# Kernel optimization log

Hardware: AMD Instinct MI355X
Metric: run time of the kernel (lower is better)

## Reference

```python
import jax, jax.numpy as jnp
import numpy as np

B, T, D_IN, H, LAT = 256, 512, 32, 128, 64


def lstm_scan(x, Wih, Whh, bih, bhh):
    """PyTorch-convention single-layer LSTM over x [B,T,D] -> hidden states [B,T,H].
    Gate order: i, f, g, o. Gates = x@Wih.T + bih + h@Whh.T + bhh."""
    Bm, _, _ = x.shape
    Hm = Whh.shape[1]
    # precompute input contributions for all timesteps: [B,T,4H]
    xg = jnp.einsum('btd,gd->btg', x, Wih) + bih + bhh

    def step(carry, g_t):
        h, c = carry
        gates = g_t + h @ Whh.T  # [B,4H]
        i, f, g, o = jnp.split(gates, 4, axis=-1)
        i = jax.nn.sigmoid(i)
        f = jax.nn.sigmoid(f)
        g = jnp.tanh(g)
        o = jax.nn.sigmoid(o)
        c = f * c + i * g
        h = o * jnp.tanh(c)
        return (h, c), h

    h0 = jnp.zeros((Bm, Hm), x.dtype)
    (_, _), hs = jax.lax.scan(step, (h0, h0), jnp.swapaxes(xg, 0, 1))
    return jnp.swapaxes(hs, 0, 1)  # [B,T,H]


def setup_inputs() -> dict:
    key = jax.random.key(0)
    ks = jax.random.split(key, 14)
    s = 1.0 / np.sqrt(H)

    def u(k, shape):
        return jax.random.uniform(k, shape, jnp.float32, -s, s)

    return {
        'x': jax.random.normal(ks[0], (B, T, D_IN), jnp.float32),
        # encoder LSTM (input_dim -> hidden)
        'enc_Wih': u(ks[1], (4 * H, D_IN)),
        'enc_Whh': u(ks[2], (4 * H, H)),
        'enc_bih': u(ks[3], (4 * H,)),
        'enc_bhh': u(ks[4], (4 * H,)),
        # encoder linear (hidden -> latent)
        'enc_Wl': u(ks[5], (LAT, H)),
        'enc_bl': u(ks[6], (LAT,)),
        # decoder LSTM (latent -> hidden)
        'dec_Wih': u(ks[7], (4 * H, LAT)),
        'dec_Whh': u(ks[8], (4 * H, H)),
        'dec_bih': u(ks[9], (4 * H,)),
        'dec_bhh': u(ks[10], (4 * H,)),
        # decoder linear (hidden -> input_dim)
        'dec_Wl': u(ks[11], (D_IN, H)),
        'dec_bl': u(ks[12], (D_IN,)),
    }


def reference(x, enc_Wih, enc_Whh, enc_bih, enc_bhh, enc_Wl, enc_bl,
              dec_Wih, dec_Whh, dec_bih, dec_bhh, dec_Wl, dec_bl):
    # Encoder: last hidden state -> linear -> latent
    hs = lstm_scan(x, enc_Wih, enc_Whh, enc_bih, enc_bhh)  # [B,T,H]
    h_last = hs[:, -1]                                     # == hidden.squeeze(0)
    encoded = h_last @ enc_Wl.T + enc_bl                   # [B,LAT]
    # Decoder: repeat latent over time, LSTM, linear
    z = jnp.broadcast_to(encoded[:, None, :], (encoded.shape[0], T, encoded.shape[1]))
    hs2 = lstm_scan(z, dec_Wih, dec_Whh, dec_bih, dec_bhh)  # [B,T,H]
    decoded = hs2 @ dec_Wl.T + dec_bl                       # [B,T,D_IN]
    return encoded, decoded
```

## Files before the change

### kernel.cpp

```cpp
#include <hip/hip_runtime.h>

#define NB   256
#define NT   512
#define NDIN 32
#define NH   128
#define NLAT 64
#define HSTR 136

typedef _Float16 f16x8 __attribute__((ext_vector_type(8)));
typedef float    f32x4 __attribute__((ext_vector_type(4)));
typedef _Float16 h2    __attribute__((ext_vector_type(2)));
typedef _Float16 h4    __attribute__((ext_vector_type(4)));

__device__ __forceinline__ float dot2(h2 a, h2 b, float c) {
  return __builtin_amdgcn_fdot2(a, b, c, false);
}
__device__ __forceinline__ h2 bc2(float v) { return __builtin_bit_cast(h2, v); }
__device__ __forceinline__ h2 pk2(float a, float b) { return h2{(_Float16)a, (_Float16)b}; }

#define NLOG2E 1.44269504f
__device__ __forceinline__ float sigmoid_f(float x) {
  return __builtin_amdgcn_rcpf(1.f + __builtin_amdgcn_exp2f(x * -NLOG2E));
}
__device__ __forceinline__ float tanh_f(float x) {
  float s = __builtin_amdgcn_rcpf(1.f + __builtin_amdgcn_exp2f(x * (-2.f * NLOG2E)));
  return fmaf(2.f, s, -1.f);
}
__device__ __forceinline__ f32x4 mfma16(f16x8 a, f16x8 b, f32x4 c) {
  return __builtin_amdgcn_mfma_f32_16x16x32_f16(a, b, c, 0, 0, 0);
}

template <int CTRL>
__device__ __forceinline__ float dpp_mov(float v) {
  int p = __builtin_amdgcn_update_dpp(0, __builtin_bit_cast(int, v),
                                      CTRL, 0xF, 0xF, true);
  return __builtin_bit_cast(float, p);
}
#define ROR4  0x124
#define ROR8  0x128
#define ROR12 0x12C

__global__ __launch_bounds__(512, 1) void lstm_ae_kernel(
    const float* __restrict__ x,
    const float* __restrict__ eWih,
    const float* __restrict__ eWhh,
    const float* __restrict__ eBih,
    const float* __restrict__ eBhh,
    const float* __restrict__ eWl,
    const float* __restrict__ eBl,
    const float* __restrict__ dWih,
    const float* __restrict__ dWhh,
    const float* __restrict__ dBih,
    const float* __restrict__ dBhh,
    const float* __restrict__ dWl,
    const float* __restrict__ dBl,
    float* __restrict__ outE,
    float* __restrict__ outD)
{
  extern __shared__ __align__(16) char smem[];
  float*    encs = (float*)smem;
  _Float16* hs   = (_Float16*)(encs + NLAT);
  _Float16* hist = hs + 2 * NH;
  _Float16* xs   = hist;
  float*    gtmp = (float*)(hist + NT * HSTR);

  const int tid = threadIdx.x;
  const int b   = blockIdx.x;
  const int w   = tid >> 6;
  const int l   = tid & 63;
  const int m   = l & 15;
  const int kg  = l >> 4;
  const int ag  = m & 3;
  const int ar  = 2 * (m >> 2);

  int au[4], cu[4];
#pragma unroll
  for (int tt = 0; tt < 4; ++tt) {
    au[tt] = 16 * w + 8 * (tt >> 1) + ar + (tt & 1);
    cu[tt] = 16 * w + 8 * (tt >> 1) + 2 * kg + (tt & 1);
  }
  const bool sb0 = (l & 1) != 0, sb1 = (l & 2) != 0;
  const bool b2  = (l & 4) != 0, b3  = (l & 8) != 0;
  const int  cu_sel = 16 * w + 8 * ((l >> 1) & 1) + 2 * kg + (l & 1);
  const bool writer = (l & 12) == 0;
  const bool gthn   = b3 && !b2;
  const float km = gthn ? (-2.f * NLOG2E) : -NLOG2E;
  const float pa = gthn ? 2.f : 1.f;
  const float pb = gthn ? -1.f : 0.f;

  {
    const float4* xg = (const float4*)(x + (size_t)b * (NT * NDIN));
    h4* xo = (h4*)xs;
#pragma unroll
    for (int i = 0; i < 8; ++i) {
      int idx = i * 512 + tid;
      float4 v = xg[idx];
      xo[idx] = h4{(_Float16)v.x, (_Float16)v.y, (_Float16)v.z, (_Float16)v.w};
    }
  }

  f16x8 aw[4][4];
  f16x8 ax[4];
  f32x4 bi[4];
#pragma unroll
  for (int tt = 0; tt < 4; ++tt) {
    const float* r = eWhh + (size_t)(ag * NH + au[tt]) * NH;
#pragma unroll
    for (int K = 0; K < 4; ++K) {
      const float* p = r + 32 * K + 8 * kg;
#pragma unroll
      for (int j = 0; j < 8; ++j) aw[tt][K][j] = (_Float16)p[j];
    }
    const float* q = eWih + (size_t)(ag * NH + au[tt]) * NDIN + 8 * kg;
#pragma unroll
    for (int j = 0; j < 8; ++j) ax[tt][j] = (_Float16)q[j];
#pragma unroll
    for (int j = 0; j < 4; ++j)
      bi[tt][j] = eBih[j * NH + cu[tt]] + eBhh[j * NH + cu[tt]];
  }
  if (tid < 2 * NH) hs[tid] = (_Float16)0.f;
  float c = 0.f;
  __syncthreads();

#pragma unroll 1
  for (int t = 0; t < NT; ++t) {
    f32x4 acc[4];
    const _Float16* hb = hs + (t & 1) * NH;
    {
      f16x8 bf = *(const f16x8*)(hb + 8 * kg);
#pragma unroll
      for (int tt = 0; tt < 4; ++tt) acc[tt] = mfma16(aw[tt][0], bf, bi[tt]);
    }
#pragma unroll
    for (int K = 1; K < 4; ++K) {
      f16x8 bf = *(const f16x8*)(hb + 32 * K + 8 * kg);
#pragma unroll
      for (int tt = 0; tt < 4; ++tt) acc[tt] = mfma16(aw[tt][K], bf, acc[tt]);
    }
    {
      f16x8 xf = *(const f16x8*)(xs + t * NDIN + 8 * kg);
#pragma unroll
      for (int tt = 0; tt < 4; ++tt) acc[tt] = mfma16(ax[tt], xf, acc[tt]);
    }
    float z;
    {
      float v0, v1, v2, v3;
      {
        float u0 = b3 ? acc[0][2] : acc[0][0], u1 = b3 ? acc[0][3] : acc[0][1];
        v0 = b2 ? u1 : u0;
      }
      {
        float u0 = b3 ? acc[1][2] : acc[1][0], u1 = b3 ? acc[1][3] : acc[1][1];
        v1 = b2 ? u1 : u0;
      }
      {
        float u0 = b3 ? acc[2][2] : acc[2][0], u1 = b3 ? acc[2][3] : acc[2][1];
        v2 = b2 ? u1 : u0;
      }
      {
        float u0 = b3 ? acc[3][2] : acc[3][0], u1 = b3 ? acc[3][3] : acc[3][1];
        v3 = b2 ? u1 : u0;
      }
      float w0 = sb1 ? v2 : v0, w1 = sb1 ? v3 : v1;
      z = sb0 ? w1 : w0;
    }
    float a = fmaf(pa, __builtin_amdgcn_rcpf(1.f + __builtin_amdgcn_exp2f(z * km)), pb);
    float vf = dpp_mov<ROR12>(a);
    float vg = dpp_mov<ROR8>(a);
    float vo = dpp_mov<ROR4>(a);
    c = fmaf(vf, c, a * vg);
    float h = vo * tanh_f(c);
    if (writer) hs[((t + 1) & 1) * NH + cu_sel] = (_Float16)h;
    __syncthreads();
  }

  if (tid < NLAT) {
    const float4* p  = (const float4*)(eWl + (size_t)tid * NH);
    const float2* hh = (const float2*)hs;
    float a = eBl[tid];
#pragma unroll
    for (int r = 0; r < 32; ++r) {
      float4 wv = p[r];
      float2 hp = hh[r];
      h2 lov = bc2(hp.x), hiv = bc2(hp.y);
      a = fmaf((float)lov.x, wv.x, a); a = fmaf((float)lov.y, wv.y, a);
      a = fmaf((float)hiv.x, wv.z, a); a = fmaf((float)hiv.y, wv.w, a);
    }
    encs[tid] = a;
    outE[b * NLAT + tid] = a;
  }
#pragma unroll
  for (int tt = 0; tt < 4; ++tt) {
    const float* r = dWhh + (size_t)(ag * NH + au[tt]) * NH;
#pragma unroll
    for (int K = 0; K < 4; ++K) {
      const float* p = r + 32 * K + 8 * kg;
#pragma unroll
      for (int j = 0; j < 8; ++j) aw[tt][K][j] = (_Float16)p[j];
    }
  }
  __syncthreads();

  if (tid < 2 * NH) hs[tid] = (_Float16)0.f;
  {
    const float4* p  = (const float4*)(dWih + (size_t)tid * NLAT);
    const float4* e4 = (const float4*)encs;
    float a = dBih[tid] + dBhh[tid];
#pragma unroll
    for (int r = 0; r < 16; ++r) {
      float4 wv = p[r]; float4 ev = e4[r];
      a = fmaf(ev.x, wv.x, a); a = fmaf(ev.y, wv.y, a);
      a = fmaf(ev.z, wv.z, a); a = fmaf(ev.w, wv.w, a);
    }
    gtmp[tid] = a;
  }
  __syncthreads();
#pragma unroll
  for (int tt = 0; tt < 4; ++tt) {
#pragma unroll
    for (int j = 0; j < 4; ++j) bi[tt][j] = gtmp[j * NH + cu[tt]];
  }
  c = 0.f;

#pragma unroll 1
  for (int t = 0; t < NT; ++t) {
    f32x4 acc[4];
    const _Float16* hb = hs + (t & 1) * NH;
    {
      f16x8 bf = *(const f16x8*)(hb + 8 * kg);
#pragma unroll
      for (int tt = 0; tt < 4; ++tt) acc[tt] = mfma16(aw[tt][0], bf, bi[tt]);
    }
#pragma unroll
    for (int K = 1; K < 4; ++K) {
      f16x8 bf = *(const f16x8*)(hb + 32 * K + 8 * kg);
#pragma unroll
      for (int tt = 0; tt < 4; ++tt) acc[tt] = mfma16(aw[tt][K], bf, acc[tt]);
    }
    float z;
    {
      float v0, v1, v2, v3;
      {
        float u0 = b3 ? acc[0][2] : acc[0][0], u1 = b3 ? acc[0][3] : acc[0][1];
        v0 = b2 ? u1 : u0;
      }
      {
        float u0 = b3 ? acc[1][2] : acc[1][0], u1 = b3 ? acc[1][3] : acc[1][1];
        v1 = b2 ? u1 : u0;
      }
      {
        float u0 = b3 ? acc[2][2] : acc[2][0], u1 = b3 ? acc[2][3] : acc[2][1];
        v2 = b2 ? u1 : u0;
      }
      {
        float u0 = b3 ? acc[3][2] : acc[3][0], u1 = b3 ? acc[3][3] : acc[3][1];
        v3 = b2 ? u1 : u0;
      }
      float w0 = sb1 ? v2 : v0, w1 = sb1 ? v3 : v1;
      z = sb0 ? w1 : w0;
    }
    float a = fmaf(pa, __builtin_amdgcn_rcpf(1.f + __builtin_amdgcn_exp2f(z * km)), pb);
    float vf = dpp_mov<ROR12>(a);
    float vg = dpp_mov<ROR8>(a);
    float vo = dpp_mov<ROR4>(a);
    c = fmaf(vf, c, a * vg);
    float h = vo * tanh_f(c);
    if (writer) {
      _Float16 hh = (_Float16)h;
      hs[((t + 1) & 1) * NH + cu_sel] = hh;
      hist[t * HSTR + cu_sel] = hh;
    }
    __syncthreads();
  }

  {
    const int col = tid & 31, rg = tid >> 5;
    h2 wl[64];
    const float4* p0 = (const float4*)(dWl + (size_t)col * NH);
#pragma unroll
    for (int f = 0; f < 32; ++f) {
      float4 v = p0[f];
      wl[2 * f] = pk2(v.x, v.y); wl[2 * f + 1] = pk2(v.z, v.w);
    }
    const float bo = dBl[col];
    float* op = outD + (size_t)b * (NT * NDIN);
#pragma unroll 1
    for (int i = 0; i < 32; ++i) {
      int r = rg + 16 * i;
      const float4* hp = (const float4*)(hist + r * HSTR);
      float s = 0.f;
#pragma unroll
      for (int j = 0; j < 16; ++j) {
        float4 hvv = hp[j];
        s = dot2(wl[4 * j + 0], bc2(hvv.x), s);
        s = dot2(wl[4 * j + 1], bc2(hvv.y), s);
        s = dot2(wl[4 * j + 2], bc2(hvv.z), s);
        s = dot2(wl[4 * j + 3], bc2(hvv.w), s);
      }
      op[(size_t)r * NDIN + col] = s + bo;
    }
  }
}

#define SMEM_BYTES (NLAT * 4 + 2 * NH * 2 + NT * HSTR * 2 + 512 * 4)

extern "C" void kernel_launch(void* const* d_in, const int* in_sizes, int n_in,
                              void* d_out, int out_size, void* d_ws, size_t ws_size,
                              hipStream_t stream) {
  const float* x    = (const float*)d_in[0];
  const float* eWih = (const float*)d_in[1];
  const float* eWhh = (const float*)d_in[2];
  const float* eBih = (const float*)d_in[3];
  const float* eBhh = (const float*)d_in[4];
  const float* eWl  = (const float*)d_in[5];
  const float* eBl  = (const float*)d_in[6];
  const float* dWih = (const float*)d_in[7];
  const float* dWhh = (const float*)d_in[8];
  const float* dBih = (const float*)d_in[9];
  const float* dBhh = (const float*)d_in[10];
  const float* dWl  = (const float*)d_in[11];
  const float* dBl  = (const float*)d_in[12];

  float* outE = (float*)d_out;
  float* outD = outE + (size_t)NB * NLAT;

  (void)hipFuncSetAttribute((const void*)lstm_ae_kernel,
                            hipFuncAttributeMaxDynamicSharedMemorySize,
                            SMEM_BYTES);

  hipLaunchKernelGGL(lstm_ae_kernel, dim3(NB), dim3(512), SMEM_BYTES, stream,
                     x, eWih, eWhh, eBih, eBhh, eWl, eBl,
                     dWih, dWhh, dBih, dBhh, dWl, dBl, outE, outD);
}
```

Measured before the change: 598.2 us.

## Replace MFMA recurrent matvec with per-thread fdot2 dot products and quad DPP reductions

Measured after the change: 625.1 us. +4.5%, slower.

```diff
diff --git a/kernel.cpp b/kernel.cpp
--- a/kernel.cpp
+++ b/kernel.cpp
@@ -7,7 +7,6 @@
 #define NLAT 64
 #define HSTR 136
 
-typedef _Float16 f16x8 __attribute__((ext_vector_type(8)));
 typedef float    f32x4 __attribute__((ext_vector_type(4)));
 typedef _Float16 h2    __attribute__((ext_vector_type(2)));
 typedef _Float16 h4    __attribute__((ext_vector_type(4)));
@@ -19,15 +18,9 @@
 __device__ __forceinline__ h2 pk2(float a, float b) { return h2{(_Float16)a, (_Float16)b}; }
 
 #define NLOG2E 1.44269504f
-__device__ __forceinline__ float sigmoid_f(float x) {
-  return __builtin_amdgcn_rcpf(1.f + __builtin_amdgcn_exp2f(x * -NLOG2E));
-}
 __device__ __forceinline__ float tanh_f(float x) {
   float s = __builtin_amdgcn_rcpf(1.f + __builtin_amdgcn_exp2f(x * (-2.f * NLOG2E)));
   return fmaf(2.f, s, -1.f);
-}
-__device__ __forceinline__ f32x4 mfma16(f16x8 a, f16x8 b, f32x4 c) {
-  return __builtin_amdgcn_mfma_f32_16x16x32_f16(a, b, c, 0, 0, 0);
 }
 
 template <int CTRL>
@@ -36,9 +29,13 @@
                                       CTRL, 0xF, 0xF, true);
   return __builtin_bit_cast(float, p);
 }
-#define ROR4  0x124
-#define ROR8  0x128
-#define ROR12 0x12C
+#define QXOR1 0xB1
+#define QXOR2 0x4E
+#define QP1   0x39
+#define QP2   0x4E
+#define QP3   0x93
+template <int CTRL>
+__device__ __forceinline__ float qadd(float v) { return v + dpp_mov<CTRL>(v); }
 
 __global__ __launch_bounds__(512, 1) void lstm_ae_kernel(
     const float* __restrict__ x,
@@ -66,27 +63,15 @@
 
   const int tid = threadIdx.x;
   const int b   = blockIdx.x;
-  const int w   = tid >> 6;
-  const int l   = tid & 63;
-  const int m   = l & 15;
-  const int kg  = l >> 4;
-  const int ag  = m & 3;
-  const int ar  = 2 * (m >> 2);
-
-  int au[4], cu[4];
-#pragma unroll
-  for (int tt = 0; tt < 4; ++tt) {
-    au[tt] = 16 * w + 8 * (tt >> 1) + ar + (tt & 1);
-    cu[tt] = 16 * w + 8 * (tt >> 1) + 2 * kg + (tt & 1);
-  }
-  const bool sb0 = (l & 1) != 0, sb1 = (l & 2) != 0;
-  const bool b2  = (l & 4) != 0, b3  = (l & 8) != 0;
-  const int  cu_sel = 16 * w + 8 * ((l >> 1) & 1) + 2 * kg + (l & 1);
-  const bool writer = (l & 12) == 0;
-  const bool gthn   = b3 && !b2;
-  const float km = gthn ? (-2.f * NLOG2E) : -NLOG2E;
-  const float pa = gthn ? 2.f : 1.f;
-  const float pb = gthn ? -1.f : 0.f;
+  const int u   = tid >> 2;
+  const int kc  = tid & 3;
+  const bool writer = (kc == 0);
+  const bool k0 = (kc & 1) != 0;
+  const bool k1 = (kc & 2) != 0;
+  const bool gth = (kc == 2);
+  const float km = gth ? (-2.f * NLOG2E) : -NLOG2E;
+  const float pa = gth ? 2.f : 1.f;
+  const float pb = gth ? -1.f : 0.f;
 
   {
     const float4* xg = (const float4*)(x + (size_t)b * (NT * NDIN));
@@ -99,24 +84,26 @@
     }
   }
 
-  f16x8 aw[4][4];
-  f16x8 ax[4];
-  f32x4 bi[4];
-#pragma unroll
-  for (int tt = 0; tt < 4; ++tt) {
-    const float* r = eWhh + (size_t)(ag * NH + au[tt]) * NH;
-#pragma unroll
-    for (int K = 0; K < 4; ++K) {
-      const float* p = r + 32 * K + 8 * kg;
-#pragma unroll
-      for (int j = 0; j < 8; ++j) aw[tt][K][j] = (_Float16)p[j];
-    }
-    const float* q = eWih + (size_t)(ag * NH + au[tt]) * NDIN + 8 * kg;
-#pragma unroll
-    for (int j = 0; j < 8; ++j) ax[tt][j] = (_Float16)q[j];
-#pragma unroll
-    for (int j = 0; j < 4; ++j)
-      bi[tt][j] = eBih[j * NH + cu[tt]] + eBhh[j * NH + cu[tt]];
+  h2 ew[64], dw[64], ewih[16];
+  float binit[4];
+#pragma unroll
+  for (int g = 0; g < 4; ++g) {
+    const int r = g * NH + u;
+    const float4* p = (const float4*)(eWhh + (size_t)r * NH + 32 * kc);
+#pragma unroll
+    for (int j = 0; j < 8; ++j) {
+      float4 v = p[j];
+      ew[g * 16 + 2 * j]     = pk2(v.x, v.y);
+      ew[g * 16 + 2 * j + 1] = pk2(v.z, v.w);
+    }
+    const float4* q = (const float4*)(eWih + (size_t)r * NDIN + 8 * kc);
+    float4 v0 = q[0], v1 = q[1];
+    ewih[g * 4 + 0] = pk2(v0.x, v0.y);
+    ewih[g * 4 + 1] = pk2(v0.z, v0.w);
+    ewih[g * 4 + 2] = pk2(v1.x, v1.y);
+    ewih[g * 4 + 3] = pk2(v1.z, v1.w);
+    float bsum = eBih[r] + eBhh[r];
+    binit[g] = writer ? bsum : 0.f;
   }
   if (tid < 2 * NH) hs[tid] = (_Float16)0.f;
   float c = 0.f;
@@ -124,53 +111,47 @@
 
 #pragma unroll 1
   for (int t = 0; t < NT; ++t) {
-    f32x4 acc[4];
-    const _Float16* hb = hs + (t & 1) * NH;
-    {
-      f16x8 bf = *(const f16x8*)(hb + 8 * kg);
-#pragma unroll
-      for (int tt = 0; tt < 4; ++tt) acc[tt] = mfma16(aw[tt][0], bf, bi[tt]);
-    }
-#pragma unroll
-    for (int K = 1; K < 4; ++K) {
-      f16x8 bf = *(const f16x8*)(hb + 32 * K + 8 * kg);
-#pragma unroll
-      for (int tt = 0; tt < 4; ++tt) acc[tt] = mfma16(aw[tt][K], bf, acc[tt]);
-    }
-    {
-      f16x8 xf = *(const f16x8*)(xs + t * NDIN + 8 * kg);
-#pragma unroll
-      for (int tt = 0; tt < 4; ++tt) acc[tt] = mfma16(ax[tt], xf, acc[tt]);
-    }
-    float z;
-    {
-      float v0, v1, v2, v3;
-      {
-        float u0 = b3 ? acc[0][2] : acc[0][0], u1 = b3 ? acc[0][3] : acc[0][1];
-        v0 = b2 ? u1 : u0;
-      }
-      {
-        float u0 = b3 ? acc[1][2] : acc[1][0], u1 = b3 ? acc[1][3] : acc[1][1];
-        v1 = b2 ? u1 : u0;
-      }
-      {
-        float u0 = b3 ? acc[2][2] : acc[2][0], u1 = b3 ? acc[2][3] : acc[2][1];
-        v2 = b2 ? u1 : u0;
-      }
-      {
-        float u0 = b3 ? acc[3][2] : acc[3][0], u1 = b3 ? acc[3][3] : acc[3][1];
-        v3 = b2 ? u1 : u0;
-      }
-      float w0 = sb1 ? v2 : v0, w1 = sb1 ? v3 : v1;
-      z = sb0 ? w1 : w0;
-    }
-    float a = fmaf(pa, __builtin_amdgcn_rcpf(1.f + __builtin_amdgcn_exp2f(z * km)), pb);
-    float vf = dpp_mov<ROR12>(a);
-    float vg = dpp_mov<ROR8>(a);
-    float vo = dpp_mov<ROR4>(a);
+    const float4* hp = (const float4*)(hs + (t & 1) * NH + 32 * kc);
+    float4 h0 = hp[0], h1 = hp[1], h2v = hp[2], h3 = hp[3];
+    float4 xv = *(const float4*)(xs + t * NDIN + 8 * kc);
+    float zz[4];
+#pragma unroll
+    for (int g = 0; g < 4; ++g) {
+      float A = binit[g];
+      A = dot2(ew[g * 16 +  0], bc2(h0.x), A);
+      A = dot2(ew[g * 16 +  1], bc2(h0.y), A);
+      A = dot2(ew[g * 16 +  2], bc2(h0.z), A);
+      A = dot2(ew[g * 16 +  3], bc2(h0.w), A);
+      A = dot2(ew[g * 16 +  4], bc2(h1.x), A);
+      A = dot2(ew[g * 16 +  5], bc2(h1.y), A);
+      A = dot2(ew[g * 16 +  6], bc2(h1.z), A);
+      A = dot2(ew[g * 16 +  7], bc2(h1.w), A);
+      A = dot2(ew[g * 16 +  8], bc2(h2v.x), A);
+      A = dot2(ew[g * 16 +  9], bc2(h2v.y), A);
+      A = dot2(ew[g * 16 + 10], bc2(h2v.z), A);
+      A = dot2(ew[g * 16 + 11], bc2(h2v.w), A);
+      A = dot2(ew[g * 16 + 12], bc2(h3.x), A);
+      A = dot2(ew[g * 16 + 13], bc2(h3.y), A);
+      A = dot2(ew[g * 16 + 14], bc2(h3.z), A);
+      A = dot2(ew[g * 16 + 15], bc2(h3.w), A);
+      A = dot2(ewih[g * 4 + 0], bc2(xv.x), A);
+      A = dot2(ewih[g * 4 + 1], bc2(xv.y), A);
+      A = dot2(ewih[g * 4 + 2], bc2(xv.z), A);
+      A = dot2(ewih[g * 4 + 3], bc2(xv.w), A);
+      A = qadd<QXOR1>(A);
+      A = qadd<QXOR2>(A);
+      zz[g] = A;
+    }
+    float zl = k0 ? zz[1] : zz[0];
+    float zh = k0 ? zz[3] : zz[2];
+    float z  = k1 ? zh : zl;
+    float a  = fmaf(pa, __builtin_amdgcn_rcpf(1.f + __builtin_amdgcn_exp2f(z * km)), pb);
+    float vf = dpp_mov<QP1>(a);
+    float vg = dpp_mov<QP2>(a);
+    float vo = dpp_mov<QP3>(a);
     c = fmaf(vf, c, a * vg);
     float h = vo * tanh_f(c);
-    if (writer) hs[((t + 1) & 1) * NH + cu_sel] = (_Float16)h;
+    if (writer) hs[((t + 1) & 1) * NH + u] = (_Float16)h;
     __syncthreads();
   }
 
@@ -190,13 +171,14 @@
     outE[b * NLAT + tid] = a;
   }
 #pragma unroll
-  for (int tt = 0; tt < 4; ++tt) {
-    const float* r = dWhh + (size_t)(ag * NH + au[tt]) * NH;
-#pragma unroll
-    for (int K = 0; K < 4; ++K) {
-      const float* p = r + 32 * K + 8 * kg;
-#pragma unroll
-      for (int j = 0; j < 8; ++j) aw[tt][K][j] = (_Float16)p[j];
+  for (int g = 0; g < 4; ++g) {
+    const int r = g * NH + u;
+    const float4* p = (const float4*)(dWhh + (size_t)r * NH + 32 * kc);
+#pragma unroll
+    for (int j = 0; j < 8; ++j) {
+      float4 v = p[j];
+      dw[g * 16 + 2 * j]     = pk2(v.x, v.y);
+      dw[g * 16 + 2 * j + 1] = pk2(v.z, v.w);
     }
   }
   __syncthreads();
@@ -215,60 +197,53 @@
     gtmp[tid] = a;
   }
   __syncthreads();
-#pragma unroll
-  for (int tt = 0; tt < 4; ++tt) {
-#pragma unroll
-    for (int j = 0; j < 4; ++j) bi[tt][j] = gtmp[j * NH + cu[tt]];
-  }
+  float dinit[4];
+#pragma unroll
+  for (int g = 0; g < 4; ++g)
+    dinit[g] = writer ? gtmp[g * NH + u] : 0.f;
   c = 0.f;
 
 #pragma unroll 1
   for (int t = 0; t < NT; ++t) {
-    f32x4 acc[4];
-    const _Float16* hb = hs + (t & 1) * NH;
-    {
-      f16x8 bf = *(const f16x8*)(hb + 8 * kg);
-#pragma unroll
-      for (int tt = 0; tt < 4; ++tt) acc[tt] = mfma16(aw[tt][0], bf, bi[tt]);
-    }
-#pragma unroll
-    for (int K = 1; K < 4; ++K) {
-      f16x8 bf = *(const f16x8*)(hb + 32 * K + 8 * kg);
-#pragma unroll
-      for (int tt = 0; tt < 4; ++tt) acc[tt] = mfma16(aw[tt][K], bf, acc[tt]);
-    }
-    float z;
-    {
-      float v0, v1, v2, v3;
-      {
-        float u0 = b3 ? acc[0][2] : acc[0][0], u1 = b3 ? acc[0][3] : acc[0][1];
-        v0 = b2 ? u1 : u0;
-      }
-      {
-        float u0 = b3 ? acc[1][2] : acc[1][0], u1 = b3 ? acc[1][3] : acc[1][1];
-        v1 = b2 ? u1 : u0;
-      }
-      {
-        float u0 = b3 ? acc[2][2] : acc[2][0], u1 = b3 ? acc[2][3] : acc[2][1];
-        v2 = b2 ? u1 : u0;
-      }
-      {
-        float u0 = b3 ? acc[3][2] : acc[3][0], u1 = b3 ? acc[3][3] : acc[3][1];
-        v3 = b2 ? u1 : u0;
-      }
-      float w0 = sb1 ? v2 : v0, w1 = sb1 ? v3 : v1;
-      z = sb0 ? w1 : w0;
-    }
-    float a = fmaf(pa, __builtin_amdgcn_rcpf(1.f + __builtin_amdgcn_exp2f(z * km)), pb);
-    float vf = dpp_mov<ROR12>(a);
-    float vg = dpp_mov<ROR8>(a);
-    float vo = dpp_mov<ROR4>(a);
+    const float4* hp = (const float4*)(hs + (t & 1) * NH + 32 * kc);
+    float4 h0 = hp[0], h1 = hp[1], h2v = hp[2], h3 = hp[3];
+    float zz[4];
+#pragma unroll
+    for (int g = 0; g < 4; ++g) {
+      float A = dinit[g];
+      A = dot2(dw[g * 16 +  0], bc2(h0.x), A);
+      A = dot2(dw[g * 16 +  1], bc2(h0.y), A);
+      A = dot2(dw[g * 16 +  2], bc2(h0.z), A);
+      A = dot2(dw[g * 16 +  3], bc2(h0.w), A);
+      A = dot2(dw[g * 16 +  4], bc2(h1.x), A);
+      A = dot2(dw[g * 16 +  5], bc2(h1.y), A);
+      A = dot2(dw[g * 16 +  6], bc2(h1.z), A);
+      A = dot2(dw[g * 16 +  7], bc2(h1.w), A);
+      A = dot2(dw[g * 16 +  8], bc2(h2v.x), A);
+      A = dot2(dw[g * 16 +  9], bc2(h2v.y), A);
+      A = dot2(dw[g * 16 + 10], bc2(h2v.z), A);
+      A = dot2(dw[g * 16 + 11], bc2(h2v.w), A);
+      A = dot2(dw[g * 16 + 12], bc2(h3.x), A);
+      A = dot2(dw[g * 16 + 13], bc2(h3.y), A);
+      A = dot2(dw[g * 16 + 14], bc2(h3.z), A);
+      A = dot2(dw[g * 16 + 15], bc2(h3.w), A);
+      A = qadd<QXOR1>(A);
+      A = qadd<QXOR2>(A);
+      zz[g] = A;
+    }
+    float zl = k0 ? zz[1] : zz[0];
+    float zh = k0 ? zz[3] : zz[2];
+    float z  = k1 ? zh : zl;
+    float a  = fmaf(pa, __builtin_amdgcn_rcpf(1.f + __builtin_amdgcn_exp2f(z * km)), pb);
+    float vf = dpp_mov<QP1>(a);
+    float vg = dpp_mov<QP2>(a);
+    float vo = dpp_mov<QP3>(a);
     c = fmaf(vf, c, a * vg);
     float h = vo * tanh_f(c);
     if (writer) {
       _Float16 hh = (_Float16)h;
-      hs[((t + 1) & 1) * NH + cu_sel] = hh;
-      hist[t * HSTR + cu_sel] = hh;
+      hs[((t + 1) & 1) * NH + u] = hh;
+      hist[t * HSTR + u] = hh;
     }
     __syncthreads();
   }
```

## Split LSTM recurrence between MFMA waves and VALU dot2 waves

Applied to the files above, without the earlier changes.

New measurement: 719.6 us. +20.3%, slower.

```diff
diff --git a/kernel.cpp b/kernel.cpp
--- a/kernel.cpp
+++ b/kernel.cpp
@@ -17,17 +17,14 @@
 }
 __device__ __forceinline__ h2 bc2(float v) { return __builtin_bit_cast(h2, v); }
 __device__ __forceinline__ h2 pk2(float a, float b) { return h2{(_Float16)a, (_Float16)b}; }
+__device__ __forceinline__ f32x4 mfma16(f16x8 a, f16x8 b, f32x4 c) {
+  return __builtin_amdgcn_mfma_f32_16x16x32_f16(a, b, c, 0, 0, 0);
+}
 
 #define NLOG2E 1.44269504f
-__device__ __forceinline__ float sigmoid_f(float x) {
-  return __builtin_amdgcn_rcpf(1.f + __builtin_amdgcn_exp2f(x * -NLOG2E));
-}
 __device__ __forceinline__ float tanh_f(float x) {
   float s = __builtin_amdgcn_rcpf(1.f + __builtin_amdgcn_exp2f(x * (-2.f * NLOG2E)));
   return fmaf(2.f, s, -1.f);
-}
-__device__ __forceinline__ f32x4 mfma16(f16x8 a, f16x8 b, f32x4 c) {
-  return __builtin_amdgcn_mfma_f32_16x16x32_f16(a, b, c, 0, 0, 0);
 }
 
 template <int CTRL>
@@ -39,6 +36,13 @@
 #define ROR4  0x124
 #define ROR8  0x128
 #define ROR12 0x12C
+#define QXOR1 0xB1
+#define QXOR2 0x4E
+#define QP1   0x39
+#define QP2   0x4E
+#define QP3   0x93
+template <int CTRL>
+__device__ __forceinline__ float qadd(float v) { return v + dpp_mov<CTRL>(v); }
 
 __global__ __launch_bounds__(512, 1) void lstm_ae_kernel(
     const float* __restrict__ x,
@@ -68,25 +72,36 @@
   const int b   = blockIdx.x;
   const int w   = tid >> 6;
   const int l   = tid & 63;
+  const bool is_mfma = (w < 4);
+
   const int m   = l & 15;
   const int kg  = l >> 4;
   const int ag  = m & 3;
   const int ar  = 2 * (m >> 2);
-
   int au[4], cu[4];
 #pragma unroll
   for (int tt = 0; tt < 4; ++tt) {
     au[tt] = 16 * w + 8 * (tt >> 1) + ar + (tt & 1);
     cu[tt] = 16 * w + 8 * (tt >> 1) + 2 * kg + (tt & 1);
   }
-  const bool sb0 = (l & 1) != 0, sb1 = (l & 2) != 0;
-  const bool b2  = (l & 4) != 0, b3  = (l & 8) != 0;
+  const bool ts0 = (l & 1) != 0, ts1 = (l & 2) != 0;
+  const bool gb2 = (l & 4) != 0, gb3 = (l & 8) != 0;
   const int  cu_sel = 16 * w + 8 * ((l >> 1) & 1) + 2 * kg + (l & 1);
-  const bool writer = (l & 12) == 0;
-  const bool gthn   = b3 && !b2;
-  const float km = gthn ? (-2.f * NLOG2E) : -NLOG2E;
-  const float pa = gthn ? 2.f : 1.f;
-  const float pb = gthn ? -1.f : 0.f;
+  const bool writer0 = (l & 12) == 0;
+  const bool gthn    = gb3 && !gb2;
+  const float km0 = gthn ? (-2.f * NLOG2E) : -NLOG2E;
+  const float pa0 = gthn ? 2.f : 1.f;
+  const float pb0 = gthn ? -1.f : 0.f;
+
+  const int u   = tid >> 2;
+  const int kc  = tid & 3;
+  const bool writer1 = (kc == 0);
+  const bool k0 = (kc & 1) != 0;
+  const bool k1 = (kc & 2) != 0;
+  const bool gthv = (kc == 2);
+  const float km1 = gthv ? (-2.f * NLOG2E) : -NLOG2E;
+  const float pa1 = gthv ? 2.f : 1.f;
+  const float pb1 = gthv ? -1.f : 0.f;
 
   {
     const float4* xg = (const float4*)(x + (size_t)b * (NT * NDIN));
@@ -102,21 +117,45 @@
   f16x8 aw[4][4];
   f16x8 ax[4];
   f32x4 bi[4];
-#pragma unroll
-  for (int tt = 0; tt < 4; ++tt) {
-    const float* r = eWhh + (size_t)(ag * NH + au[tt]) * NH;
-#pragma unroll
-    for (int K = 0; K < 4; ++K) {
-      const float* p = r + 32 * K + 8 * kg;
-#pragma unroll
-      for (int j = 0; j < 8; ++j) aw[tt][K][j] = (_Float16)p[j];
-    }
-    const float* q = eWih + (size_t)(ag * NH + au[tt]) * NDIN + 8 * kg;
-#pragma unroll
-    for (int j = 0; j < 8; ++j) ax[tt][j] = (_Float16)q[j];
-#pragma unroll
-    for (int j = 0; j < 4; ++j)
-      bi[tt][j] = eBih[j * NH + cu[tt]] + eBhh[j * NH + cu[tt]];
+  h2 ew[64], ewih[16];
+  float binit[4];
+  if (is_mfma) {
+#pragma unroll
+    for (int tt = 0; tt < 4; ++tt) {
+      const float* r = eWhh + (size_t)(ag * NH + au[tt]) * NH;
+#pragma unroll
+      for (int K = 0; K < 4; ++K) {
+        const float* p = r + 32 * K + 8 * kg;
+#pragma unroll
+        for (int j = 0; j < 8; ++j) aw[tt][K][j] = (_Float16)p[j];
+      }
+      const float* q = eWih + (size_t)(ag * NH + au[tt]) * NDIN + 8 * kg;
+#pragma unroll
+      for (int j = 0; j < 8; ++j) ax[tt][j] = (_Float16)q[j];
+#pragma unroll
+      for (int j = 0; j < 4; ++j)
+        bi[tt][j] = eBih[j * NH + cu[tt]] + eBhh[j * NH + cu[tt]];
+    }
+  } else {
+#pragma unroll
+    for (int g = 0; g < 4; ++g) {
+      const int r = g * NH + u;
+      const float4* p = (const float4*)(eWhh + (size_t)r * NH + 32 * kc);
+#pragma unroll
+      for (int j = 0; j < 8; ++j) {
+        float4 v = p[j];
+        ew[g * 16 + 2 * j]     = pk2(v.x, v.y);
+        ew[g * 16 + 2 * j + 1] = pk2(v.z, v.w);
+      }
+      const float4* q = (const float4*)(eWih + (size_t)r * NDIN + 8 * kc);
+      float4 v0 = q[0], v1 = q[1];
+      ewih[g * 4 + 0] = pk2(v0.x, v0.y);
+      ewih[g * 4 + 1] = pk2(v0.z, v0.w);
+      ewih[g * 4 + 2] = pk2(v1.x, v1.y);
+      ewih[g * 4 + 3] = pk2(v1.z, v1.w);
+      float bsum = eBih[r] + eBhh[r];
+      binit[g] = writer1 ? bsum : 0.f;
+    }
   }
   if (tid < 2 * NH) hs[tid] = (_Float16)0.f;
   float c = 0.f;
@@ -124,53 +163,85 @@
 
 #pragma unroll 1
   for (int t = 0; t < NT; ++t) {
-    f32x4 acc[4];
     const _Float16* hb = hs + (t & 1) * NH;
-    {
-      f16x8 bf = *(const f16x8*)(hb + 8 * kg);
-#pragma unroll
-      for (int tt = 0; tt < 4; ++tt) acc[tt] = mfma16(aw[tt][0], bf, bi[tt]);
-    }
-#pragma unroll
-    for (int K = 1; K < 4; ++K) {
-      f16x8 bf = *(const f16x8*)(hb + 32 * K + 8 * kg);
-#pragma unroll
-      for (int tt = 0; tt < 4; ++tt) acc[tt] = mfma16(aw[tt][K], bf, acc[tt]);
-    }
-    {
-      f16x8 xf = *(const f16x8*)(xs + t * NDIN + 8 * kg);
-#pragma unroll
-      for (int tt = 0; tt < 4; ++tt) acc[tt] = mfma16(ax[tt], xf, acc[tt]);
-    }
-    float z;
-    {
-      float v0, v1, v2, v3;
+    if (is_mfma) {
+      f32x4 acc[4];
       {
-        float u0 = b3 ? acc[0][2] : acc[0][0], u1 = b3 ? acc[0][3] : acc[0][1];
-        v0 = b2 ? u1 : u0;
+        f16x8 bf = *(const f16x8*)(hb + 8 * kg);
+#pragma unroll
+        for (int tt = 0; tt < 4; ++tt) acc[tt] = mfma16(aw[tt][0], bf, bi[tt]);
+      }
+#pragma unroll
+      for (int K = 1; K < 4; ++K) {
+        f16x8 bf = *(const f16x8*)(hb + 32 * K + 8 * kg);
+#pragma unroll
+        for (int tt = 0; tt < 4; ++tt) acc[tt] = mfma16(aw[tt][K], bf, acc[tt]);
       }
       {
-        float u0 = b3 ? acc[1][2] : acc[1][0], u1 = b3 ? acc[1][3] : acc[1][1];
-        v1 = b2 ? u1 : u0;
-      }
+        f16x8 xf = *(const f16x8*)(xs + t * NDIN + 8 * kg);
+#pragma unroll
+        for (int tt = 0; tt < 4; ++tt) acc[tt] = mfma16(ax[tt], xf, acc[tt]);
+      }
+      float z;
       {
-        float u0 = b3 ? acc[2][2] : acc[2][0], u1 = b3 ? acc[2][3] : acc[2][1];
-        v2 = b2 ? u1 : u0;
-      }
-      {
-        float u0 = b3 ? acc[3][2] : acc[3][0], u1 = b3 ? acc[3][3] : acc[3][1];
-        v3 = b2 ? u1 : u0;
-      }
-      float w0 = sb1 ? v2 : v0, w1 = sb1 ? v3 : v1;
-      z = sb0 ? w1 : w0;
-    }
-    float a = fmaf(pa, __builtin_amdgcn_rcpf(1.f + __builtin_amdgcn_exp2f(z * km)), pb);
-    float vf = dpp_mov<ROR12>(a);
-    float vg = dpp_mov<ROR8>(a);
-    float vo = dpp_mov<ROR4>(a);
-    c = fmaf(vf, c, a * vg);
-    float h = vo * tanh_f(c);
-    if (writer) hs[((t + 1) & 1) * NH + cu_sel] = (_Float16)h;
+        float v0, v1, v2, v3;
+        { float u0 = gb3 ? acc[0][2] : acc[0][0], u1 = gb3 ? acc[0][3] : acc[0][1]; v0 = gb2 ? u1 : u0; }
+        { float u0 = gb3 ? acc[1][2] : acc[1][0], u1 = gb3 ? acc[1][3] : acc[1][1]; v1 = gb2 ? u1 : u0; }
+        { float u0 = gb3 ? acc[2][2] : acc[2][0], u1 = gb3 ? acc[2][3] : acc[2][1]; v2 = gb2 ? u1 : u0; }
+        { float u0 = gb3 ? acc[3][2] : acc[3][0], u1 = gb3 ? acc[3][3] : acc[3][1]; v3 = gb2 ? u1 : u0; }
+        float w0 = ts1 ? v2 : v0, w1 = ts1 ? v3 : v1;
+        z = ts0 ? w1 : w0;
+      }
+      float a = fmaf(pa0, __builtin_amdgcn_rcpf(1.f + __builtin_amdgcn_exp2f(z * km0)), pb0);
+      float vf = dpp_mov<ROR12>(a);
+      float vg = dpp_mov<ROR8>(a);
+      float vo = dpp_mov<ROR4>(a);
+      c = fmaf(vf, c, a * vg);
+      float h = vo * tanh_f(c);
+      if (writer0) hs[((t + 1) & 1) * NH + cu_sel] = (_Float16)h;
+    } else {
+      const float4* hp = (const float4*)(hb + 32 * kc);
+      float4 h0 = hp[0], h1 = hp[1], h2v = hp[2], h3 = hp[3];
+      float4 xv = *(const float4*)(xs + t * NDIN + 8 * kc);
+      float zz[4];
+#pragma unroll
+      for (int g = 0; g < 4; ++g) {
+        float A = binit[g];
+        A = dot2(ew[g * 16 +  0], bc2(h0.x), A);
+        A = dot2(ew[g * 16 +  1], bc2(h0.y), A);
+        A = dot2(ew[g * 16 +  2], bc2(h0.z), A);
+        A = dot2(ew[g * 16 +  3], bc2(h0.w), A);
+        A = dot2(ew[g * 16 +  4], bc2(h1.x), A);
+        A = dot2(ew[g * 16 +  5], bc2(h1.y), A);
+        A = dot2(ew[g * 16 +  6], bc2(h1.z), A);
+        A = dot2(ew[g * 16 +  7], bc2(h1.w), A);
+        A = dot2(ew[g * 16 +  8], bc2(h2v.x), A);
+        A = dot2(ew[g * 16 +  9], bc2(h2v.y), A);
+        A = dot2(ew[g * 16 + 10], bc2(h2v.z), A);
+        A = dot2(ew[g * 16 + 11], bc2(h2v.w), A);
+        A = dot2(ew[g * 16 + 12], bc2(h3.x), A);
+        A = dot2(ew[g * 16 + 13], bc2(h3.y), A);
+        A = dot2(ew[g * 16 + 14], bc2(h3.z), A);
+        A = dot2(ew[g * 16 + 15], bc2(h3.w), A);
+        A = dot2(ewih[g * 4 + 0], bc2(xv.x), A);
+        A = dot2(ewih[g * 4 + 1], bc2(xv.y), A);
+        A = dot2(ewih[g * 4 + 2], bc2(xv.z), A);
+        A = dot2(ewih[g * 4 + 3], bc2(xv.w), A);
+        A = qadd<QXOR1>(A);
+        A = qadd<QXOR2>(A);
+        zz[g] = A;
+      }
+      float zl = k0 ? zz[1] : zz[0];
+      float zh = k0 ? zz[3] : zz[2];
+      float z  = k1 ? zh : zl;
+      float a  = fmaf(pa1, __builtin_amdgcn_rcpf(1.f + __builtin_amdgcn_exp2f(z * km1)), pb1);
+      float vf = dpp_mov<QP1>(a);
+      float vg = dpp_mov<QP2>(a);
+      float vo = dpp_mov<QP3>(a);
+      c = fmaf(vf, c, a * vg);
+      float h = vo * tanh_f(c);
+      if (writer1) hs[((t + 1) & 1) * NH + u] = (_Float16)h;
+    }
     __syncthreads();
   }
 
@@ -189,14 +260,28 @@
     encs[tid] = a;
     outE[b * NLAT + tid] = a;
   }
-#pragma unroll
-  for (int tt = 0; tt < 4; ++tt) {
-    const float* r = dWhh + (size_t)(ag * NH + au[tt]) * NH;
-#pragma unroll
-    for (int K = 0; K < 4; ++K) {
-      const float* p = r + 32 * K + 8 * kg;
-#pragma unroll
-      for (int j = 0; j < 8; ++j) aw[tt][K][j] = (_Float16)p[j];
+  if (is_mfma) {
+#pragma unroll
+    for (int tt = 0; tt < 4; ++tt) {
+      const float* r = dWhh + (size_t)(ag * NH + au[tt]) * NH;
+#pragma unroll
+      for (int K = 0; K < 4; ++K) {
+        const float* p = r + 32 * K + 8 * kg;
+#pragma unroll
+        for (int j = 0; j < 8; ++j) aw[tt][K][j] = (_Float16)p[j];
+      }
+    }
+  } else {
+#pragma unroll
+    for (int g = 0; g < 4; ++g) {
+      const int r = g * NH + u;
+      const float4* p = (const float4*)(dWhh + (size_t)r * NH + 32 * kc);
+#pragma unroll
+      for (int j = 0; j < 8; ++j) {
+        float4 v = p[j];
+        ew[g * 16 + 2 * j]     = pk2(v.x, v.y);
+        ew[g * 16 + 2 * j + 1] = pk2(v.z, v.w);
+      }
     }
   }
   __syncthreads();
@@ -215,60 +300,98 @@
     gtmp[tid] = a;
   }
   __syncthreads();
-#pragma unroll
-  for (int tt = 0; tt < 4; ++tt) {
-#pragma unroll
-    for (int j = 0; j < 4; ++j) bi[tt][j] = gtmp[j * NH + cu[tt]];
+  float dinit[4];
+  if (is_mfma) {
+#pragma unroll
+    for (int tt = 0; tt < 4; ++tt) {
+#pragma unroll
+      for (int j = 0; j < 4; ++j) bi[tt][j] = gtmp[j * NH + cu[tt]];
+    }
+  } else {
+#pragma unroll
+    for (int g = 0; g < 4; ++g)
+      dinit[g] = writer1 ? gtmp[g * NH + u] : 0.f;
   }
   c = 0.f;
 
 #pragma unroll 1
   for (int t = 0; t < NT; ++t) {
-    f32x4 acc[4];
     const _Float16* hb = hs + (t & 1) * NH;
-    {
-      f16x8 bf = *(const f16x8*)(hb + 8 * kg);
-#pragma unroll
-      for (int tt = 0; tt < 4; ++tt) acc[tt] = mfma16(aw[tt][0], bf, bi[tt]);
-    }
-#pragma unroll
-    for (int K = 1; K < 4; ++K) {
-      f16x8 bf = *(const f16x8*)(hb + 32 * K + 8 * kg);
-#pragma unroll
-      for (int tt = 0; tt < 4; ++tt) acc[tt] = mfma16(aw[tt][K], bf, acc[tt]);
-    }
-    float z;
-    {
-      float v0, v1, v2, v3;
+    if (is_mfma) {
+      f32x4 acc[4];
       {
-        float u0 = b3 ? acc[0][2] : acc[0][0], u1 = b3 ? acc[0][3] : acc[0][1];
-        v0 = b2 ? u1 : u0;
-      }
+        f16x8 bf = *(const f16x8*)(hb + 8 * kg);
+#pragma unroll
+        for (int tt = 0; tt < 4; ++tt) acc[tt] = mfma16(aw[tt][0], bf, bi[tt]);
+      }
+#pragma unroll
+      for (int K = 1; K < 4; ++K) {
+        f16x8 bf = *(const f16x8*)(hb + 32 * K + 8 * kg);
+#pragma unroll
+        for (int tt = 0; tt < 4; ++tt) acc[tt] = mfma16(aw[tt][K], bf, acc[tt]);
+      }
+      float z;
       {
-        float u0 = b3 ? acc[1][2] : acc[1][0], u1 = b3 ? acc[1][3] : acc[1][1];
-        v1 = b2 ? u1 : u0;
-      }
-      {
-        float u0 = b3 ? acc[2][2] : acc[2][0], u1 = b3 ? acc[2][3] : acc[2][1];
-        v2 = b2 ? u1 : u0;
-      }
-      {
-        float u0 = b3 ? acc[3][2] : acc[3][0], u1 = b3 ? acc[3][3] : acc[3][1];
-        v3 = b2 ? u1 : u0;
-      }
-      float w0 = sb1 ? v2 : v0, w1 = sb1 ? v3 : v1;
-      z = sb0 ? w1 : w0;
-    }
-    float a = fmaf(pa, __builtin_amdgcn_rcpf(1.f + __builtin_amdgcn_exp2f(z * km)), pb);
-    float vf = dpp_mov<ROR12>(a);
-    float vg = dpp_mov<ROR8>(a);
-    float vo = dpp_mov<ROR4>(a);
-    c = fmaf(vf, c, a * vg);
-    float h = vo * tanh_f(c);
-    if (writer) {
-      _Float16 hh = (_Float16)h;
-      hs[((t + 1) & 1) * NH + cu_sel] = hh;
-      hist[t * HSTR + cu_sel] = hh;
+        float v0, v1, v2, v3;
+        { float u0 = gb3 ? acc[0][2] : acc[0][0], u1 = gb3 ? acc[0][3] : acc[0][1]; v0 = gb2 ? u1 : u0; }
+        { float u0 = gb3 ? acc[1][2] : acc[1][0], u1 = gb3 ? acc[1][3] : acc[1][1]; v1 = gb2 ? u1 : u0; }
+        { float u0 = gb3 ? acc[2][2] : acc[2][0], u1 = gb3 ? acc[2][3] : acc[2][1]; v2 = gb2 ? u1 : u0; }
+        { float u0 = gb3 ? acc[3][2] : acc[3][0], u1 = gb3 ? acc[3][3] : acc[3][1]; v3 = gb2 ? u1 : u0; }
+        float w0 = ts1 ? v2 : v0, w1 = ts1 ? v3 : v1;
+        z = ts0 ? w1 : w0;
+      }
+      float a = fmaf(pa0, __builtin_amdgcn_rcpf(1.f + __builtin_amdgcn_exp2f(z * km0)), pb0);
+      float vf = dpp_mov<ROR12>(a);
+      float vg = dpp_mov<ROR8>(a);
+      float vo = dpp_mov<ROR4>(a);
+      c = fmaf(vf, c, a * vg);
+      float h = vo * tanh_f(c);
+      if (writer0) {
+        _Float16 hh = (_Float16)h;
+        hs[((t + 1) & 1) * NH + cu_sel] = hh;
+        hist[t * HSTR + cu_sel] = hh;
+      }
+    } else {
+      const float4* hp = (const float4*)(hb + 32 * kc);
+      float4 h0 = hp[0], h1 = hp[1], h2v = hp[2], h3 = hp[3];
+      float zz[4];
+#pragma unroll
+      for (int g = 0; g < 4; ++g) {
+        float A = dinit[g];
+        A = dot2(ew[g * 16 +  0], bc2(h0.x), A);
+        A = dot2(ew[g * 16 +  1], bc2(h0.y), A);
+        A = dot2(ew[g * 16 +  2], bc2(h0.z), A);
+        A = dot2(ew[g * 16 +  3], bc2(h0.w), A);
+        A = dot2(ew[g * 16 +  4], bc2(h1.x), A);
+        A = dot2(ew[g * 16 +  5], bc2(h1.y), A);
+        A = dot2(ew[g * 16 +  6], bc2(h1.z), A);
+        A = dot2(ew[g * 16 +  7], bc2(h1.w), A);
+        A = dot2(ew[g * 16 +  8], bc2(h2v.x), A);
+        A = dot2(ew[g * 16 +  9], bc2(h2v.y), A);
+        A = dot2(ew[g * 16 + 10], bc2(h2v.z), A);
+        A = dot2(ew[g * 16 + 11], bc2(h2v.w), A);
+        A = dot2(ew[g * 16 + 12], bc2(h3.x), A);
+        A = dot2(ew[g * 16 + 13], bc2(h3.y), A);
+        A = dot2(ew[g * 16 + 14], bc2(h3.z), A);
+        A = dot2(ew[g * 16 + 15], bc2(h3.w), A);
+        A = qadd<QXOR1>(A);
+        A = qadd<QXOR2>(A);
+        zz[g] = A;
+      }
+      float zl = k0 ? zz[1] : zz[0];
+      float zh = k0 ? zz[3] : zz[2];
+      float z  = k1 ? zh : zl;
+      float a  = fmaf(pa1, __builtin_amdgcn_rcpf(1.f + __builtin_amdgcn_exp2f(z * km1)), pb1);
+      float vf = dpp_mov<QP1>(a);
+      float vg = dpp_mov<QP2>(a);
+      float vo = dpp_mov<QP3>(a);
+      c = fmaf(vf, c, a * vg);
+      float h = vo * tanh_f(c);
+      if (writer1) {
+        _Float16 hh = (_Float16)h;
+        hs[((t + 1) & 1) * NH + u] = hh;
+        hist[t * HSTR + u] = hh;
+      }
     }
     __syncthreads();
   }
```
